# Kernel optimization log

Measured on AMD Instinct MI355X. Metric: run time of the kernel, lower is better.

The kernel has to match this reference:

```python
import jax, jax.numpy as jnp
import numpy as np

B, S, D, H = 2, 2048, 1024, 16
HD = D // H  # 64


def setup_inputs() -> dict:
    key = jax.random.key(0)
    k0, k1, k2 = jax.random.split(key, 3)
    return {
        "x": jax.random.normal(k0, (B, S, D), jnp.float32),
        "qkv_w": jax.random.normal(k1, (D, 3 * D), jnp.float32) / np.sqrt(D).astype(np.float32),
        "qkv_b": jnp.zeros((3 * D,), jnp.float32),
        "out_w": jax.random.normal(k2, (D, D), jnp.float32) / np.sqrt(D).astype(np.float32),
        "out_b": jnp.zeros((D,), jnp.float32),
    }


def reference(x, qkv_w, qkv_b, out_w, out_b):
    b, s, d = x.shape
    h, hd = H, d // H
    scale = 1.0 / np.sqrt(hd).astype(np.float32)
    # qkv projection: [b, s, 3d] -> [b, s, 3, h, hd]
    qkv = (x @ qkv_w + qkv_b).reshape(b, s, 3, h, hd)
    q, k, v = qkv[:, :, 0], qkv[:, :, 1], qkv[:, :, 2]  # each [b, s, h, hd]
    # attention logits [b, h, q, k]
    logits = jnp.einsum("bqhd,bkhd->bhqk", q, k)
    # causal mask applied before scaling (as in source; -inf is scale-invariant)
    causal_mask = jnp.triu(jnp.ones((s, s), bool), 1)
    logits = jnp.where(causal_mask, -jnp.inf, logits) * scale
    att = jax.nn.softmax(logits, axis=-1)
    out = jnp.einsum("bhqk,bkhd->bqhd", att, v).reshape(b, s, d)
    return out @ out_w + out_b
```

## Files before the change

### kernel.cpp

```cpp
#include <hip/hip_runtime.h>


typedef __bf16 bf16x8 __attribute__((ext_vector_type(8)));
typedef float f32x4 __attribute__((ext_vector_type(4)));
typedef float f32x16 __attribute__((ext_vector_type(16)));
typedef unsigned short u16;
typedef u16 u16x8 __attribute__((ext_vector_type(8)));
typedef unsigned u32x4 __attribute__((ext_vector_type(4)));

#define QSCALE 0.180336880110323f
#define FIXED_M 24.0f

__device__ __forceinline__ u16 f2b(float f) {
    unsigned u = __builtin_bit_cast(unsigned, f);
    u += 0x7fffu + ((u >> 16) & 1u);
    return (u16)(u >> 16);
}

__device__ __forceinline__ unsigned cvtpk(float lo, float hi) {
    unsigned r;
    asm("v_cvt_pk_bf16_f32 %0, %1, %2" : "=v"(r) : "v"(lo), "v"(hi));
    return r;
}

__device__ __forceinline__ void plswap(unsigned &a, unsigned &b) {
    asm("v_permlane32_swap_b32 %0, %1" : "+v"(a), "+v"(b));
}

__device__ __forceinline__ void gload_lds16(const u16* g, u16* l) {
    __builtin_amdgcn_global_load_lds(
        (__attribute__((address_space(1))) unsigned int*)(g),
        (__attribute__((address_space(3))) unsigned int*)(l),
        16u, 0, 0u);
}

__device__ __forceinline__ int swzb(int u) {
    return u ^ (((u >> 7) & 7) << 4);
}

__global__ void cast_f32_bf16(const float* __restrict__ X, u16* __restrict__ Y, int n4)
{
    int i = blockIdx.x * blockDim.x + threadIdx.x;
    if (i >= n4) return;
    float4 v = ((const float4*)X)[i];
    ((ushort4*)Y)[i] = make_ushort4(f2b(v.x), f2b(v.y), f2b(v.z), f2b(v.w));
}

__global__ void transpose_cast(const float* __restrict__ W, u16* __restrict__ Wt, int K, int N)
{
    __shared__ float tile[32][33];
    const int c0 = blockIdx.x * 32, r0 = blockIdx.y * 32;
    const int tc = threadIdx.x & 31, tr = threadIdx.x >> 5;
#pragma unroll
    for (int i = 0; i < 4; ++i)
        tile[tr + i*8][tc] = W[(size_t)(r0 + tr + i*8) * N + c0 + tc];
    __syncthreads();
#pragma unroll
    for (int i = 0; i < 4; ++i) {
        int nn = tr + i*8;
        Wt[(size_t)(c0 + nn) * K + r0 + tc] = f2b(tile[tc][nn]);
    }
}

__global__ __launch_bounds__(256) void gemm_qkv(
    const u16* __restrict__ A, const u16* __restrict__ Bt,
    const float* __restrict__ bias,
    u16* __restrict__ qb, u16* __restrict__ kb, u16* __restrict__ vt,
    int M, int N, int K)
{
    __shared__ __align__(16) u16 smem[16384];
    u16* As = smem;
    u16* Bs = smem + 8192;
    const int tid  = threadIdx.x;
    const int wave = tid >> 6, lane = tid & 63;
    const int quad = lane >> 4, l16 = lane & 15;
    const int m0 = blockIdx.y * 128, n0 = blockIdx.x * 128;
    const int wm = (wave >> 1) * 64, wn = (wave & 1) * 64;

    f32x4 acc[4][4] = {};

    auto stage = [&](int buf, int kt) {
#pragma unroll
        for (int iss = 0; iss < 2; ++iss) {
            const int e = iss * 2048 + tid * 8;
            const int row = e >> 5, col = e & 31;
            gload_lds16(A  + (size_t)(m0 + row) * K + kt + col, As + buf*4096 + iss*2048 + wave*512);
            gload_lds16(Bt + (size_t)(n0 + row) * K + kt + col, Bs + buf*4096 + iss*2048 + wave*512);
        }
    };

    stage(0, 0);
    __syncthreads();

    int buf = 0;
    for (int kt = 0; kt < K; kt += 32) {
        if (kt + 32 < K) stage(buf ^ 1, kt + 32);

        bf16x8 af[4], bfr[4];
#pragma unroll
        for (int i = 0; i < 4; ++i) {
            af[i]  = *(const bf16x8*)(As + buf*4096 + (wm + i*16 + l16) * 32 + quad * 8);
            bfr[i] = *(const bf16x8*)(Bs + buf*4096 + (wn + i*16 + l16) * 32 + quad * 8);
        }
#pragma unroll
        for (int i = 0; i < 4; ++i)
#pragma unroll
            for (int j = 0; j < 4; ++j)
                acc[i][j] = __builtin_amdgcn_mfma_f32_16x16x32_bf16(af[i], bfr[j], acc[i][j], 0, 0, 0);
        __syncthreads();
        buf ^= 1;
    }

    if (n0 >= 2048) {
        const int b = m0 >> 11, s0 = m0 & 2047;
        u16* TT = smem;
#pragma unroll
        for (int hh = 0; hh < 2; ++hh) {
            if ((wave & 1) == hh) {
#pragma unroll
                for (int j = 0; j < 4; ++j) {
                    const int hd = j*16 + l16;
                    const float bv = bias[n0 + wn + j*16 + l16];
#pragma unroll
                    for (int i = 0; i < 4; ++i) {
                        const int sl = wm + i*16 + quad*4;
                        ushort4 w = make_ushort4(
                            f2b(acc[i][j][0] + bv), f2b(acc[i][j][1] + bv),
                            f2b(acc[i][j][2] + bv), f2b(acc[i][j][3] + bv));
                        *(ushort4*)(&TT[hd*136 + sl]) = w;
                    }
                }
            }
            __syncthreads();
            const int h = ((n0 + hh*64) >> 6) & 15;
            u16* dst = vt + ((size_t)(b*16 + h)) * (64 * 2048) + s0;
            const int rr = tid >> 4, cc = (tid & 15) * 8;
#pragma unroll
            for (int it = 0; it < 4; ++it) {
                const int row = it*16 + rr;
                u16x8 v = *(const u16x8*)(&TT[row*136 + cc]);
                *(u16x8*)(dst + (size_t)row * 2048 + cc) = v;
            }
            __syncthreads();
        }
        return;
    }

#pragma unroll
    for (int i = 0; i < 4; ++i)
#pragma unroll
        for (int j = 0; j < 4; ++j)
#pragma unroll
            for (int r = 0; r < 4; ++r) {
                const int m = m0 + wm + i*16 + quad*4 + r;
                const int n = n0 + wn + j*16 + l16;
                float v = acc[i][j][r] + bias[n];
                const int t = n >> 10, h = (n >> 6) & 15, hd = n & 63;
                const int b = m >> 11, s = m & 2047;
                const size_t idx = ((size_t)(b * 16 + h) * 2048 + s) * 64 + hd;
                if (t == 0)      qb[idx] = f2b(v * QSCALE);
                else             kb[idx] = f2b(v);
            }
}

__global__ __launch_bounds__(256) void gemm_proj(
    const u16* __restrict__ A, const u16* __restrict__ Bt,
    const float* __restrict__ bias, float* __restrict__ Cf,
    int M, int N, int K)
{
    __shared__ __align__(16) u16 As[2][128 * 32];
    __shared__ __align__(16) u16 Bs[2][128 * 32];
    const int tid  = threadIdx.x;
    const int wave = tid >> 6, lane = tid & 63;
    const int quad = lane >> 4, l16 = lane & 15;

    const int nx = gridDim.x, nwg = nx * gridDim.y;
    int wg = blockIdx.y * nx + blockIdx.x;
    wg = (wg & 7) * (nwg >> 3) + (wg >> 3);
    const int m0 = (wg / nx) * 128, n0 = (wg % nx) * 128;
    const int wm = (wave >> 1) * 64, wn = (wave & 1) * 64;

    f32x4 acc[4][4] = {};

    auto stage = [&](int buf, int kt) {
#pragma unroll
        for (int iss = 0; iss < 2; ++iss) {
            const int e = iss * 2048 + tid * 8;
            const int row = e >> 5, col = e & 31;
            gload_lds16(A  + (size_t)(m0 + row) * K + kt + col, &As[buf][iss * 2048 + wave * 512]);
            gload_lds16(Bt + (size_t)(n0 + row) * K + kt + col, &Bs[buf][iss * 2048 + wave * 512]);
        }
    };

    stage(0, 0);
    __syncthreads();

    int buf = 0;
    for (int kt = 0; kt < K; kt += 32) {
        if (kt + 32 < K) stage(buf ^ 1, kt + 32);

        bf16x8 af[4], bfr[4];
#pragma unroll
        for (int i = 0; i < 4; ++i) {
            af[i]  = *(const bf16x8*)(&As[buf][(wm + i*16 + l16) * 32 + quad * 8]);
            bfr[i] = *(const bf16x8*)(&Bs[buf][(wn + i*16 + l16) * 32 + quad * 8]);
        }
#pragma unroll
        for (int i = 0; i < 4; ++i)
#pragma unroll
            for (int j = 0; j < 4; ++j)
                acc[i][j] = __builtin_amdgcn_mfma_f32_16x16x32_bf16(af[i], bfr[j], acc[i][j], 0, 0, 0);
        __syncthreads();
        buf ^= 1;
    }

#pragma unroll
    for (int i = 0; i < 4; ++i)
#pragma unroll
        for (int j = 0; j < 4; ++j)
#pragma unroll
            for (int r = 0; r < 4; ++r) {
                const int m = m0 + wm + i*16 + quad*4 + r;
                const int n = n0 + wn + j*16 + l16;
                Cf[(size_t)m * N + n] = acc[i][j][r] + bias[n];
            }
}

__global__ __launch_bounds__(256) void flash_attn(
    const u16* __restrict__ qb, const u16* __restrict__ kb, const u16* __restrict__ vt,
    u16* __restrict__ attn)
{
    __shared__ __align__(16) u16 Kl[2][4096];
    __shared__ __align__(16) u16 Vl[2][4096];
    __shared__ float red_f[2][2][2][16][64];
    __shared__ float red_li[2][2][64];
    __shared__ float al[2][2][32];

    const int tid  = threadIdx.x;
    const int wave = tid >> 6, lane = tid & 63;
    const int l31 = lane & 31, hi = lane >> 5;
    const int hi8 = hi * 8, hi4 = hi * 4;

    const int lin = (int)blockIdx.x;
    const int bh  = 2*(lin & 7) + ((lin >> 3) & 1) + 16*((lin >> 4) & 1);
    const int g   = lin >> 5;
    const int pairsel = wave >> 1, phase = wave & 1;
    const int p   = 2 * g + pairsel;
    const size_t base = (size_t)bh * (2048 * 64);

    const int rb0 = 32 * p;
    const int rb1 = 32 * (63 - p);
    const int klo = p, khi = 63 - p;
    const int T = 32 - g;

    int koff[2], voff[2], dstw[2];
#pragma unroll
    for (int i = 0; i < 2; ++i) {
        const int u = (tid + 256 * i) * 16;
        const int ktsub = u >> 12, krow = (u >> 7) & 31;
        koff[i] = (ktsub * 32 + krow) * 64 + ((u & 127) >> 1);
        const int half = (u >> 6) & 1;
        voff[i] = (krow * 2 + half) * 2048 + ktsub * 32 + ((u & 63) >> 1);
        dstw[i] = swzb(u) >> 1;
    }
    int rdK[4], rdV[2][2];
#pragma unroll
    for (int ks = 0; ks < 4; ++ks) {
        const int u = phase * 4096 + l31 * 128 + ks * 32 + hi * 16;
        rdK[ks] = swzb(u) >> 1;
    }
#pragma unroll
    for (int c = 0; c < 2; ++c)
#pragma unroll
        for (int s2 = 0; s2 < 2; ++s2) {
            const int u = phase * 4096 + (c * 16 + (l31 >> 1)) * 128 + (l31 & 1) * 64
                        + s2 * 32 + hi * 16;
            rdV[c][s2] = swzb(u) >> 1;
        }

    bf16x8 qf[2][4];
#pragma unroll
    for (int ks = 0; ks < 4; ++ks) {
        qf[0][ks] = *(const bf16x8*)(qb + base + (size_t)(rb0 + l31) * 64 + ks*16 + hi8);
        qf[1][ks] = *(const bf16x8*)(qb + base + (size_t)(rb1 + l31) * 64 + ks*16 + hi8);
    }

    f32x16 minit;
#pragma unroll
    for (int r = 0; r < 16; ++r) minit[r] = -FIXED_M;

    f32x16 of[2][2] = {};
    float li[2] = {0.f, 0.f};

    u16x8 rk[2], rv[2];
    auto LOADS = [&](int s) {
#pragma unroll
        for (int i = 0; i < 2; ++i) {
            rk[i] = *(const u16x8*)(kb + base + (size_t)s * 4096 + koff[i]);
            rv[i] = *(const u16x8*)(vt + base + (size_t)s * 64 + voff[i]);
        }
    };
    auto WRITES = [&](int b) {
#pragma unroll
        for (int i = 0; i < 2; ++i) {
            *(u16x8*)(&Kl[b][dstw[i]]) = rk[i];
            *(u16x8*)(&Vl[b][dstw[i]]) = rv[i];
        }
    };

    LOADS(0); WRITES(0);
    __syncthreads();

    for (int s = 0; s < T; ++s) {
        const bool pre = (s + 1 < T);
        if (pre) LOADS(s + 1);

        const int kth = 2 * s + phase;
        const int key0 = kth * 32;
        const bool a_hi = (kth <= khi), a_lo = (kth <= klo);

        if (a_hi | a_lo) {
            const int buf = s & 1;
            bf16x8 kf[4], vf[2][2];
#pragma unroll
            for (int ks = 0; ks < 4; ++ks)
                kf[ks] = *(const bf16x8*)(&Kl[buf][rdK[ks]]);
#pragma unroll
            for (int c = 0; c < 2; ++c)
#pragma unroll
                for (int s2 = 0; s2 < 2; ++s2)
                    vf[c][s2] = *(const bf16x8*)(&Vl[buf][rdV[c][s2]]);

#define PROC_TILE(TT, RB, MT)                                                    \
        do {                                                                     \
            __builtin_amdgcn_s_setprio(1);                                       \
            f32x16 st = __builtin_amdgcn_mfma_f32_32x32x16_bf16(kf[0], qf[TT][0], minit, 0, 0, 0); \
            _Pragma("unroll")                                                    \
            for (int ks = 1; ks < 4; ++ks)                                       \
                st = __builtin_amdgcn_mfma_f32_32x32x16_bf16(kf[ks], qf[TT][ks], st, 0, 0, 0); \
            __builtin_amdgcn_s_setprio(0);                                       \
            const bool mt_ = (MT);                                               \
            const int lim_ = (RB) + l31 - key0;                                  \
            _Pragma("unroll")                                                    \
            for (int r = 0; r < 16; ++r) {                                       \
                float e = __builtin_exp2f(st[r]);                                \
                if (mt_ && ((r&3) + 8*(r>>2) + hi4 > lim_)) e = 0.f;             \
                st[r] = e;                                                       \
            }                                                                    \
            li[TT] += (((st[0]+st[1]) + (st[2]+st[3])) + ((st[4]+st[5]) + (st[6]+st[7]))) \
                    + (((st[8]+st[9]) + (st[10]+st[11])) + ((st[12]+st[13]) + (st[14]+st[15]))); \
            unsigned cw[8];                                                      \
            _Pragma("unroll")                                                    \
            for (int i = 0; i < 8; ++i) cw[i] = cvtpk(st[2*i], st[2*i+1]);       \
            plswap(cw[0], cw[2]); plswap(cw[1], cw[3]);                          \
            plswap(cw[4], cw[6]); plswap(cw[5], cw[7]);                          \
            bf16x8 pa[2];                                                        \
            { u32x4 t0 = {cw[0], cw[1], cw[2], cw[3]};                           \
              u32x4 t1 = {cw[4], cw[5], cw[6], cw[7]};                           \
              pa[0] = __builtin_bit_cast(bf16x8, t0);                            \
              pa[1] = __builtin_bit_cast(bf16x8, t1); }                          \
            __builtin_amdgcn_s_setprio(1);                                       \
            _Pragma("unroll")                                                    \
            for (int c = 0; c < 2; ++c) {                                        \
                of[TT][c] = __builtin_amdgcn_mfma_f32_32x32x16_bf16(pa[0], vf[c][0], of[TT][c], 0, 0, 0); \
                of[TT][c] = __builtin_amdgcn_mfma_f32_32x32x16_bf16(pa[1], vf[c][1], of[TT][c], 0, 0, 0); \
            }                                                                    \
            __builtin_amdgcn_s_setprio(0);                                       \
        } while (0)

            if (a_hi) PROC_TILE(1, rb1, kth == khi);
            if (a_lo) PROC_TILE(0, rb0, kth == klo);
#undef PROC_TILE
        }

        if (pre) WRITES((s + 1) & 1);
        __syncthreads();
    }

    if (phase) {
#pragma unroll
        for (int t = 0; t < 2; ++t) {
#pragma unroll
            for (int c = 0; c < 2; ++c)
#pragma unroll
                for (int i = 0; i < 16; ++i)
                    red_f[pairsel][t][c][i][lane] = of[t][c][i];
            red_li[pairsel][t][lane] = li[t];
        }
    }
    __syncthreads();
    if (phase) return;
#pragma unroll
    for (int t = 0; t < 2; ++t) {
#pragma unroll
        for (int c = 0; c < 2; ++c)
#pragma unroll
            for (int i = 0; i < 16; ++i)
                of[t][c][i] += red_f[pairsel][t][c][i][lane];
        li[t] += red_li[pairsel][t][lane];
    }

#pragma unroll
    for (int t = 0; t < 2; ++t) {
        li[t] += __shfl_xor(li[t], 32);
        al[pairsel][t][l31] = li[t];
    }
    const int b = bh >> 4, h = bh & 15;
    const int rbs[2] = {rb0, rb1};
#pragma unroll
    for (int t = 0; t < 2; ++t)
#pragma unroll
        for (int gq = 0; gq < 4; ++gq) {
            const f32x4 lv = *(const f32x4*)(&al[pairsel][t][gq*8 + hi4]);
            f32x4 inv;
#pragma unroll
            for (int rr = 0; rr < 4; ++rr) inv[rr] = 1.0f / lv[rr];
#pragma unroll
            for (int c = 0; c < 2; ++c)
#pragma unroll
                for (int rr = 0; rr < 4; ++rr) {
                    const int q = rbs[t] + gq*8 + hi4 + rr;
                    u16* dst = attn + ((size_t)(b * 2048 + q)) * 1024 + h * 64 + c*32;
                    dst[l31] = f2b(of[t][c][gq*4 + rr] * inv[rr]);
                }
        }
}

extern "C" void kernel_launch(void* const* d_in, const int* in_sizes, int n_in,
                              void* d_out, int out_size, void* d_ws, size_t ws_size,
                              hipStream_t stream)
{
    const float* x     = (const float*)d_in[0];
    const float* qkv_w = (const float*)d_in[1];
    const float* qkv_b = (const float*)d_in[2];
    const float* out_w = (const float*)d_in[3];
    const float* out_b = (const float*)d_in[4];
    float* out = (float*)d_out;

    char* ws = (char*)d_ws;
    u16* qkv_wt = (u16*)ws;  ws += (size_t)3072 * 1024 * 2;
    u16* out_wt = (u16*)ws;  ws += (size_t)1024 * 1024 * 2;
    u16* xb     = (u16*)ws;  ws += (size_t)4096 * 1024 * 2;
    u16* qb     = (u16*)ws;  ws += (size_t)4096 * 1024 * 2;
    u16* kb     = (u16*)ws;  ws += (size_t)4096 * 1024 * 2;
    u16* vt     = (u16*)ws;

    cast_f32_bf16<<<4096, 256, 0, stream>>>(x, xb, 4096 * 1024 / 4);
    transpose_cast<<<dim3(96, 32), 256, 0, stream>>>(qkv_w, qkv_wt, 1024, 3072);
    transpose_cast<<<dim3(32, 32), 256, 0, stream>>>(out_w, out_wt, 1024, 1024);

    gemm_qkv<<<dim3(24, 32), 256, 0, stream>>>(xb, qkv_wt, qkv_b, qb, kb, vt,
                                               4096, 3072, 1024);
    flash_attn<<<512, 256, 0, stream>>>(qb, kb, vt, xb);
    gemm_proj<<<dim3(8, 32), 256, 0, stream>>>(xb, out_wt, out_b, out, 4096, 1024, 1024);
}
```

Before: 195.4 us.

## Triple-buffer GEMM LDS staging with one barrier per k-step and MFMA priority

Both GEMM kernels move from a double-buffered loop with a trailing __syncthreads to a three-stage ring of LDS buffers. Each k-step waits only until the oldest in-flight loads land (vmcnt(4)), then issues a single barrier. Each step prefetches two tiles ahead and raises wave priority around the MFMA block, so global-to-LDS latency overlaps compute better and barrier stalls drop. The cost is 50% more LDS per block, which may reduce occupancy, plus redundant reloads of the last tile at the tail.

Result: faster. 181.3 us (-7.2%).

```diff
diff --git a/kernel.cpp b/kernel.cpp
--- a/kernel.cpp
+++ b/kernel.cpp
@@ -62,15 +62,40 @@
     }
 }
 
+#define GEMM_PIPE_LOOP(NST)                                                       \
+    stage(0, 0); stage(1, 32);                                                    \
+    for (int t = 0; t < (NST); ++t) {                                             \
+        asm volatile("s_waitcnt vmcnt(4)" ::: "memory");                          \
+        __builtin_amdgcn_s_barrier();                                             \
+        __builtin_amdgcn_sched_barrier(0);                                        \
+        const u16* Ab = smem + (t % 3) * 8192;                                    \
+        const u16* Bb = Ab + 4096;                                                \
+        bf16x8 af[4], bfr[4];                                                     \
+        _Pragma("unroll")                                                         \
+        for (int i = 0; i < 4; ++i) {                                             \
+            af[i]  = *(const bf16x8*)(Ab + (wm + i*16 + l16) * 32 + quad * 8);    \
+            bfr[i] = *(const bf16x8*)(Bb + (wn + i*16 + l16) * 32 + quad * 8);    \
+        }                                                                         \
+        const int tn = (t + 2 < (NST)) ? t + 2 : (NST) - 1;                       \
+        stage((t + 2) % 3, tn * 32);                                              \
+        __builtin_amdgcn_s_setprio(1);                                            \
+        _Pragma("unroll")                                                         \
+        for (int i = 0; i < 4; ++i)                                               \
+            _Pragma("unroll")                                                     \
+            for (int j = 0; j < 4; ++j)                                           \
+                acc[i][j] = __builtin_amdgcn_mfma_f32_16x16x32_bf16(              \
+                    af[i], bfr[j], acc[i][j], 0, 0, 0);                           \
+        __builtin_amdgcn_s_setprio(0);                                            \
+    }                                                                             \
+    asm volatile("s_waitcnt vmcnt(0)" ::: "memory");
+
 __global__ __launch_bounds__(256) void gemm_qkv(
     const u16* __restrict__ A, const u16* __restrict__ Bt,
     const float* __restrict__ bias,
     u16* __restrict__ qb, u16* __restrict__ kb, u16* __restrict__ vt,
     int M, int N, int K)
 {
-    __shared__ __align__(16) u16 smem[16384];
-    u16* As = smem;
-    u16* Bs = smem + 8192;
+    __shared__ __align__(16) u16 smem[3 * 8192];
     const int tid  = threadIdx.x;
     const int wave = tid >> 6, lane = tid & 63;
     const int quad = lane >> 4, l16 = lane & 15;
@@ -79,39 +104,21 @@
 
     f32x4 acc[4][4] = {};
 
-    auto stage = [&](int buf, int kt) {
+    auto stage = [&](int sb, int kt) {
+        u16* base = smem + sb * 8192;
 #pragma unroll
         for (int iss = 0; iss < 2; ++iss) {
             const int e = iss * 2048 + tid * 8;
             const int row = e >> 5, col = e & 31;
-            gload_lds16(A  + (size_t)(m0 + row) * K + kt + col, As + buf*4096 + iss*2048 + wave*512);
-            gload_lds16(Bt + (size_t)(n0 + row) * K + kt + col, Bs + buf*4096 + iss*2048 + wave*512);
+            gload_lds16(A  + (size_t)(m0 + row) * K + kt + col, base + iss*2048 + wave*512);
+            gload_lds16(Bt + (size_t)(n0 + row) * K + kt + col, base + 4096 + iss*2048 + wave*512);
         }
     };
 
-    stage(0, 0);
-    __syncthreads();
-
-    int buf = 0;
-    for (int kt = 0; kt < K; kt += 32) {
-        if (kt + 32 < K) stage(buf ^ 1, kt + 32);
-
-        bf16x8 af[4], bfr[4];
-#pragma unroll
-        for (int i = 0; i < 4; ++i) {
-            af[i]  = *(const bf16x8*)(As + buf*4096 + (wm + i*16 + l16) * 32 + quad * 8);
-            bfr[i] = *(const bf16x8*)(Bs + buf*4096 + (wn + i*16 + l16) * 32 + quad * 8);
-        }
-#pragma unroll
-        for (int i = 0; i < 4; ++i)
-#pragma unroll
-            for (int j = 0; j < 4; ++j)
-                acc[i][j] = __builtin_amdgcn_mfma_f32_16x16x32_bf16(af[i], bfr[j], acc[i][j], 0, 0, 0);
+    GEMM_PIPE_LOOP(32)
+
+    if (n0 >= 2048) {
         __syncthreads();
-        buf ^= 1;
-    }
-
-    if (n0 >= 2048) {
         const int b = m0 >> 11, s0 = m0 & 2047;
         u16* TT = smem;
 #pragma unroll
@@ -168,8 +175,7 @@
     const float* __restrict__ bias, float* __restrict__ Cf,
     int M, int N, int K)
 {
-    __shared__ __align__(16) u16 As[2][128 * 32];
-    __shared__ __align__(16) u16 Bs[2][128 * 32];
+    __shared__ __align__(16) u16 smem[3 * 8192];
     const int tid  = threadIdx.x;
     const int wave = tid >> 6, lane = tid & 63;
     const int quad = lane >> 4, l16 = lane & 15;
@@ -182,37 +188,18 @@
 
     f32x4 acc[4][4] = {};
 
-    auto stage = [&](int buf, int kt) {
+    auto stage = [&](int sb, int kt) {
+        u16* base = smem + sb * 8192;
 #pragma unroll
         for (int iss = 0; iss < 2; ++iss) {
             const int e = iss * 2048 + tid * 8;
             const int row = e >> 5, col = e & 31;
-            gload_lds16(A  + (size_t)(m0 + row) * K + kt + col, &As[buf][iss * 2048 + wave * 512]);
-            gload_lds16(Bt + (size_t)(n0 + row) * K + kt + col, &Bs[buf][iss * 2048 + wave * 512]);
+            gload_lds16(A  + (size_t)(m0 + row) * K + kt + col, base + iss*2048 + wave*512);
+            gload_lds16(Bt + (size_t)(n0 + row) * K + kt + col, base + 4096 + iss*2048 + wave*512);
         }
     };
 
-    stage(0, 0);
-    __syncthreads();
-
-    int buf = 0;
-    for (int kt = 0; kt < K; kt += 32) {
-        if (kt + 32 < K) stage(buf ^ 1, kt + 32);
-
-        bf16x8 af[4], bfr[4];
-#pragma unroll
-        for (int i = 0; i < 4; ++i) {
-            af[i]  = *(const bf16x8*)(&As[buf][(wm + i*16 + l16) * 32 + quad * 8]);
-            bfr[i] = *(const bf16x8*)(&Bs[buf][(wn + i*16 + l16) * 32 + quad * 8]);
-        }
-#pragma unroll
-        for (int i = 0; i < 4; ++i)
-#pragma unroll
-            for (int j = 0; j < 4; ++j)
-                acc[i][j] = __builtin_amdgcn_mfma_f32_16x16x32_bf16(af[i], bfr[j], acc[i][j], 0, 0, 0);
-        __syncthreads();
-        buf ^= 1;
-    }
+    GEMM_PIPE_LOOP(32)
 
 #pragma unroll
     for (int i = 0; i < 4; ++i)
```
